# Kernel tuning notes

Hardware: AMD Instinct MI355X
Metric: run time of the kernel (lower is better)

## Reference

```python
import jax, jax.numpy as jnp
import numpy as np

NEG_SLOPE = 0.2
LN_EPS = 1e-5


def gat_conv(x, edge_index, W, att_src, att_dst, bias, heads, out_ch, concat):
    """PyG-style GATConv with add_self_loops=True, eval mode (no dropout)."""
    N = x.shape[0]
    loop = jnp.arange(N, dtype=edge_index.dtype)
    src = jnp.concatenate([edge_index[0], loop])
    dst = jnp.concatenate([edge_index[1], loop])
    h = (x @ W).reshape(N, heads, out_ch)                      # [N,H,C]
    a_src = jnp.sum(h * att_src, axis=-1)                      # [N,H]
    a_dst = jnp.sum(h * att_dst, axis=-1)                      # [N,H]
    e = jax.nn.leaky_relu(a_src[src] + a_dst[dst], NEG_SLOPE)  # [E,H]
    emax = jax.ops.segment_max(e, dst, num_segments=N)         # [N,H]
    ex = jnp.exp(e - emax[dst])
    denom = jax.ops.segment_sum(ex, dst, num_segments=N)       # [N,H]
    alpha = ex / denom[dst]                                    # [E,H]
    msg = h[src] * alpha[..., None]                            # [E,H,C]
    out = jax.ops.segment_sum(msg, dst, num_segments=N)        # [N,H,C]
    out = out.reshape(N, heads * out_ch) if concat else out.mean(axis=1)
    return out + bias


def layer_norm(x, w, b):
    mu = x.mean(-1, keepdims=True)
    var = jnp.mean((x - mu) ** 2, -1, keepdims=True)
    return (x - mu) * jax.lax.rsqrt(var + LN_EPS) * w + b


def setup_inputs() -> dict:
    key = jax.random.key(0)
    ks = jax.random.split(key, 16)
    N, E, R = 50000, 800000, 16
    node_dim, res_dim, hidden, heads = 128, 64, 64, 2
    s = lambda fan: 1.0 / np.sqrt(fan)
    return {
        "x": jax.random.normal(ks[0], (N, node_dim), jnp.float32),
        "edge_index": jax.random.randint(ks[1], (2, E), 0, N, jnp.int64),
        "resource_features": jax.random.normal(ks[2], (N, R, res_dim), jnp.float32),
        "W1": jax.random.normal(ks[3], (node_dim, heads * hidden), jnp.float32) * s(node_dim),
        "att_src1": jax.random.normal(ks[4], (heads, hidden), jnp.float32) * s(hidden),
        "att_dst1": jax.random.normal(ks[5], (heads, hidden), jnp.float32) * s(hidden),
        "b1": jnp.zeros((heads * hidden,), jnp.float32),
        "W2": jax.random.normal(ks[6], (heads * hidden, hidden), jnp.float32) * s(heads * hidden),
        "att_src2": jax.random.normal(ks[7], (1, hidden), jnp.float32) * s(hidden),
        "att_dst2": jax.random.normal(ks[8], (1, hidden), jnp.float32) * s(hidden),
        "b2": jnp.zeros((hidden,), jnp.float32),
        "ln_w": jnp.ones((hidden,), jnp.float32),
        "ln_b": jnp.zeros((hidden,), jnp.float32),
        "res_W": jax.random.normal(ks[9], (res_dim, hidden), jnp.float32) * s(res_dim),
        "res_b": jnp.zeros((hidden,), jnp.float32),
    }


def reference(x, edge_index, resource_features, W1, att_src1, att_dst1, b1,
              W2, att_src2, att_dst2, b2, ln_w, ln_b, res_W, res_b):
    hidden = W2.shape[1]
    heads = att_src1.shape[0]
    h = jax.nn.elu(gat_conv(x, edge_index, W1, att_src1, att_dst1, b1,
                            heads, hidden, concat=True))
    h = gat_conv(h, edge_index, W2, att_src2, att_dst2, b2,
                 1, hidden, concat=False)
    h = layer_norm(h, ln_w, ln_b)                              # [N, hidden]
    R = resource_features.shape[1]
    x_expanded = jnp.broadcast_to(h[:, None, :], (h.shape[0], R, hidden))
    res_emb = jax.nn.elu(resource_features @ res_W + res_b)    # [N,R,hidden]
    return jnp.concatenate([x_expanded, res_emb], axis=-1)     # [N,R,2*hidden]
```

## Files before the change

kernel.cpp:

```cpp
#include <hip/hip_runtime.h>
#include <hip/hip_bf16.h>
#include <math.h>

#define LEAKY_SLOPE 0.2f
#define LN_EPS 1e-5f

typedef __attribute__((ext_vector_type(4))) float f32x4;
typedef __attribute__((ext_vector_type(8))) short short8;

__device__ __forceinline__ float leaky_relu(float x) { return x >= 0.f ? x : LEAKY_SLOPE * x; }
__device__ __forceinline__ float elu1(float x) { return x > 0.f ? x : expm1f(x); }
__device__ __forceinline__ short f2bf(float f) {
    union { __hip_bfloat16 b; short s; } u;
    u.b = __float2bfloat16(f);
    return u.s;
}
__device__ __forceinline__ float bflo(unsigned u) { union { unsigned i; float f; } x; x.i = u << 16; return x.f; }
__device__ __forceinline__ float bfhi(unsigned u) { union { unsigned i; float f; } x; x.i = u & 0xffff0000u; return x.f; }
__device__ __forceinline__ float sbf(short s) { union { unsigned i; float f; } x; x.i = ((unsigned)(unsigned short)s) << 16; return x.f; }
__device__ __forceinline__ unsigned fkey(float f) {
    unsigned b = __float_as_uint(f);
    return b ^ (unsigned)(((int)b >> 31) | 0x80000000);
}
__device__ __forceinline__ float funkey(unsigned k) {
    unsigned b = (k & 0x80000000u) ? (k ^ 0x80000000u) : ~k;
    return __uint_as_float(b);
}

#define DETECT_IS64(ei, E)                                              \
    __shared__ int s_is64;                                              \
    {                                                                   \
        if (threadIdx.x < 64) {                                         \
            int v = (threadIdx.x < (E)) ? ((const int*)(ei))[2 * threadIdx.x + 1] : 0; \
            unsigned long long b = __ballot(v != 0);                    \
            if (threadIdx.x == 0) s_is64 = (b == 0ULL);                 \
        }                                                               \
        __syncthreads();                                                \
    }

#define SUBW1 130
#define DEGB 512
__global__ __launch_bounds__(256) void k_fat1(
    const float* __restrict__ x, const float* __restrict__ W1,
    const float* __restrict__ att_s, const float* __restrict__ att_d,
    short* __restrict__ h1, float* __restrict__ a_src, float* __restrict__ a_dst,
    unsigned* __restrict__ amax, int N,
    const void* __restrict__ ei, int E, int* __restrict__ deg, int nbG)
{
    if ((int)blockIdx.x >= nbG) {
        DETECT_IS64(ei, E)
        const int is64 = s_is64;
        const int b0 = (int)blockIdx.x - nbG;
        for (int e = b0 * 256 + threadIdx.x; e < E; e += DEGB * 256) {
            int d = is64 ? (int)((const long long*)ei)[(size_t)E + e] : ((const int*)ei)[(size_t)E + e];
            atomicAdd(&deg[d], 1);
        }
        return;
    }
    __shared__ short WT[16 * SUBW1 * 8];
    __shared__ float sb[64 * 4];
    __shared__ float wm[8];
    const int t = threadIdx.x;
    const int w = t >> 6, l = t & 63, lr = l & 15, lk = l >> 4;
    const int n0 = blockIdx.x * 64;
    for (int idx = t; idx < 16384; idx += 256) {
        int k = idx >> 7, col = idx & 127;
        WT[((k >> 3) * SUBW1 + col) * 8 + (k & 7)] = f2bf(W1[idx]);
    }
    sb[t] = 0.f;
    __syncthreads();

    f32x4 acc[4][2];
    #pragma unroll
    for (int mt = 0; mt < 4; ++mt)
        #pragma unroll
        for (int nt = 0; nt < 2; ++nt) acc[mt][nt] = (f32x4){0.f, 0.f, 0.f, 0.f};

    #pragma unroll
    for (int ks = 0; ks < 4; ++ks) {
        short8 bfr[2];
        #pragma unroll
        for (int nt = 0; nt < 2; ++nt) {
            int col = w * 32 + nt * 16 + lr;
            int kk = ks * 4 + lk;
            bfr[nt] = *(const short8*)&WT[(kk * SUBW1 + col) * 8];
        }
        #pragma unroll
        for (int mt = 0; mt < 4; ++mt) {
            int row = n0 + mt * 16 + lr; if (row >= N) row = N - 1;
            const float* ap = x + (size_t)row * 128 + ks * 32 + lk * 8;
            float4 u0 = *(const float4*)ap;
            float4 u1 = *(const float4*)(ap + 4);
            short8 af;
            af[0] = f2bf(u0.x); af[1] = f2bf(u0.y); af[2] = f2bf(u0.z); af[3] = f2bf(u0.w);
            af[4] = f2bf(u1.x); af[5] = f2bf(u1.y); af[6] = f2bf(u1.z); af[7] = f2bf(u1.w);
            acc[mt][0] = __builtin_amdgcn_mfma_f32_16x16x32_bf16(af, bfr[0], acc[mt][0], 0, 0, 0);
            acc[mt][1] = __builtin_amdgcn_mfma_f32_16x16x32_bf16(af, bfr[1], acc[mt][1], 0, 0, 0);
        }
    }

    const int head = w >> 1;
    float asv[2], adv[2];
    #pragma unroll
    for (int nt = 0; nt < 2; ++nt) {
        int ci = (w & 1) * 32 + nt * 16 + lr;
        asv[nt] = att_s[head * 64 + ci];
        adv[nt] = att_d[head * 64 + ci];
    }
    #pragma unroll
    for (int mt = 0; mt < 4; ++mt) {
        #pragma unroll
        for (int i = 0; i < 4; ++i) {
            float ps = acc[mt][0][i] * asv[0] + acc[mt][1][i] * asv[1];
            float pd = acc[mt][0][i] * adv[0] + acc[mt][1][i] * adv[1];
            #pragma unroll
            for (int o = 1; o < 16; o <<= 1) { ps += __shfl_xor(ps, o); pd += __shfl_xor(pd, o); }
            int rl = mt * 16 + lk * 4 + i;
            if (lr == 0) {
                atomicAdd(&sb[rl * 4 + head], ps);
                atomicAdd(&sb[rl * 4 + 2 + head], pd);
            }
            int row = n0 + rl;
            if (row < N) {
                h1[(size_t)row * 128 + w * 32 + lr]      = f2bf(acc[mt][0][i]);
                h1[(size_t)row * 128 + w * 32 + 16 + lr] = f2bf(acc[mt][1][i]);
            }
        }
    }
    __syncthreads();
    int nl = t >> 2, q = t & 3, n = n0 + nl;
    float v = sb[t];
    bool ok = (n < N);
    if (ok) {
        if (q == 0) a_src[n * 2 + 0] = v;
        else if (q == 1) a_src[n * 2 + 1] = v;
        else if (q == 2) a_dst[n * 2 + 0] = v;
        else a_dst[n * 2 + 1] = v;
    }
    float m0 = (ok && q == 0) ? v : -1e30f;
    float m1 = (ok && q == 1) ? v : -1e30f;
    #pragma unroll
    for (int o = 32; o; o >>= 1) { m0 = fmaxf(m0, __shfl_xor(m0, o)); m1 = fmaxf(m1, __shfl_xor(m1, o)); }
    if (l == 0) { wm[w] = m0; wm[4 + w] = m1; }
    __syncthreads();
    if (t == 0) {
        float M0 = fmaxf(fmaxf(wm[0], wm[1]), fmaxf(wm[2], wm[3]));
        float M1 = fmaxf(fmaxf(wm[4], wm[5]), fmaxf(wm[6], wm[7]));
        atomicMax(&amax[0], fkey(M0));
        atomicMax(&amax[1], fkey(M1));
    }
}

__global__ __launch_bounds__(256) void k_bsum(const int* __restrict__ deg, int* __restrict__ bsum, int n)
{
    __shared__ int ws[4];
    const int base = blockIdx.x * 1024;
    int s = 0;
    for (int j = threadIdx.x; j < 1024; j += 256) {
        int i = base + j;
        s += (i < n) ? deg[i] : 0;
    }
    #pragma unroll
    for (int o = 32; o; o >>= 1) s += __shfl_down(s, o);
    if ((threadIdx.x & 63) == 0) ws[threadIdx.x >> 6] = s;
    __syncthreads();
    if (threadIdx.x == 0) bsum[blockIdx.x] = ws[0] + ws[1] + ws[2] + ws[3];
}

__global__ void k_scanb(const int* __restrict__ bsum, int* __restrict__ bbase, int nb)
{
    const int l = threadIdx.x;
    int carry = 0;
    for (int b = 0; b < nb; b += 64) {
        int v = (b + l < nb) ? bsum[b + l] : 0;
        int x = v;
        #pragma unroll
        for (int o = 1; o < 64; o <<= 1) { int y = __shfl_up(x, o); if (l >= o) x += y; }
        if (b + l < nb) bbase[b + l] = carry + x - v;
        carry += __shfl(x, 63);
    }
}

__global__ __launch_bounds__(1024) void k_scan3(const int* __restrict__ deg, const int* __restrict__ bbase,
                                                int* __restrict__ offs, int* __restrict__ cursor, int n)
{
    __shared__ int ws[16];
    const int i = blockIdx.x * 1024 + threadIdx.x;
    const int l = threadIdx.x & 63, w = threadIdx.x >> 6;
    int v = (i < n) ? deg[i] : 0;
    int x = v;
    #pragma unroll
    for (int o = 1; o < 64; o <<= 1) { int y = __shfl_up(x, o); if (l >= o) x += y; }
    if (l == 63) ws[w] = x;
    __syncthreads();
    if (threadIdx.x < 16) {
        int s = ws[threadIdx.x];
        #pragma unroll
        for (int o = 1; o < 16; o <<= 1) { int y = __shfl_up(s, o); if (threadIdx.x >= o) s += y; }
        ws[threadIdx.x] = s;
    }
    __syncthreads();
    int add = (w ? ws[w - 1] : 0) + bbase[blockIdx.x];
    if (i < n) {
        offs[i + 1] = x + add;
        cursor[i] = x + add - v;
    }
    if (blockIdx.x == 0 && threadIdx.x == 0) offs[0] = 0;
}

__global__ __launch_bounds__(256) void k_scatter(const void* __restrict__ ei, int E,
                                                 int* __restrict__ cursor, int* __restrict__ csr_src)
{
    DETECT_IS64(ei, E)
    const int is64 = s_is64;
    for (int e = blockIdx.x * blockDim.x + threadIdx.x; e < E; e += gridDim.x * blockDim.x) {
        int s, d;
        if (is64) {
            const long long* p = (const long long*)ei;
            s = (int)p[e]; d = (int)p[(size_t)E + e];
        } else {
            const int* p = (const int*)ei;
            s = p[e]; d = p[(size_t)E + e];
        }
        int pos = atomicAdd(&cursor[d], 1);
        csr_src[pos] = s;
    }
}

__global__ __launch_bounds__(256) void k_layer1(
    const short* __restrict__ h1, const float* __restrict__ a_s, const float* __restrict__ a_d,
    const int* __restrict__ offs, const int* __restrict__ csr,
    const float* __restrict__ b1, const unsigned* __restrict__ amax,
    short* __restrict__ h1a, int N)
{
    const int w = threadIdx.x >> 6, l = threadIdx.x & 63;
    const int n = blockIdx.x * 4 + w;
    if (n >= N) return;
    const float2 adp = *(const float2*)&a_d[2 * n];
    const float2 asp = *(const float2*)&a_s[2 * n];
    const float C0 = leaky_relu(funkey(amax[0]) + adp.x);
    const float C1 = leaky_relu(funkey(amax[1]) + adp.y);
    const float es0 = leaky_relu(asp.x + adp.x) - C0;
    const float es1 = leaky_relu(asp.y + adp.y) - C1;
    const int hsel = l >> 5;
    const int o0 = offs[n], o1 = offs[n + 1];

    float den0 = 0.f, den1 = 0.f;
    float cl0 = 0.f, ch0 = 0.f, cl1 = 0.f, ch1 = 0.f;
    float cl2 = 0.f, ch2 = 0.f, cl3 = 0.f, ch3 = 0.f;
    for (int base = o0; base < o1; base += 64) {
        const int cnt = min(64, o1 - base);
        int sidx = 0; float p0 = 0.f, p1 = 0.f;
        if (l < cnt) {
            sidx = csr[base + l];
            float2 av = *(const float2*)&a_s[2 * sidx];
            p0 = __expf(leaky_relu(av.x + adp.x) - C0);
            p1 = __expf(leaky_relu(av.y + adp.y) - C1);
        }
        den0 += p0; den1 += p1;
        int j = 0;
        for (; j + 4 <= cnt; j += 4) {
            int s0 = __shfl(sidx, j),     s1 = __shfl(sidx, j + 1);
            int s2 = __shfl(sidx, j + 2), s3 = __shfl(sidx, j + 3);
            float q00 = __shfl(p0, j),     q10 = __shfl(p1, j);
            float q01 = __shfl(p0, j + 1), q11 = __shfl(p1, j + 1);
            float q02 = __shfl(p0, j + 2), q12 = __shfl(p1, j + 2);
            float q03 = __shfl(p0, j + 3), q13 = __shfl(p1, j + 3);
            unsigned u0 = *(const unsigned*)(h1 + (size_t)s0 * 128 + 2 * l);
            unsigned u1 = *(const unsigned*)(h1 + (size_t)s1 * 128 + 2 * l);
            unsigned u2 = *(const unsigned*)(h1 + (size_t)s2 * 128 + 2 * l);
            unsigned u3 = *(const unsigned*)(h1 + (size_t)s3 * 128 + 2 * l);
            float w0 = hsel ? q10 : q00, w1 = hsel ? q11 : q01;
            float w2 = hsel ? q12 : q02, w3 = hsel ? q13 : q03;
            cl0 += w0 * bflo(u0); ch0 += w0 * bfhi(u0);
            cl1 += w1 * bflo(u1); ch1 += w1 * bfhi(u1);
            cl2 += w2 * bflo(u2); ch2 += w2 * bfhi(u2);
            cl3 += w3 * bflo(u3); ch3 += w3 * bfhi(u3);
        }
        for (; j < cnt; ++j) {
            int sa = __shfl(sidx, j);
            float qa0 = __shfl(p0, j), qa1 = __shfl(p1, j);
            unsigned ua = *(const unsigned*)(h1 + (size_t)sa * 128 + 2 * l);
            float wa = hsel ? qa1 : qa0;
            cl0 += wa * bflo(ua); ch0 += wa * bfhi(ua);
        }
    }
    #pragma unroll
    for (int o = 32; o; o >>= 1) { den0 += __shfl_xor(den0, o); den1 += __shfl_xor(den1, o); }
    const float psf0 = __expf(es0), psf1 = __expf(es1);
    const float inv0 = 1.f / (den0 + psf0), inv1 = 1.f / (den1 + psf1);

    unsigned us = *(const unsigned*)(h1 + (size_t)n * 128 + 2 * l);
    const float psf = hsel ? psf1 : psf0;
    float acc0 = cl0 + cl1 + cl2 + cl3 + psf * bflo(us);
    float acc1 = ch0 + ch1 + ch2 + ch3 + psf * bfhi(us);
    const float invh = hsel ? inv1 : inv0;
    float2 bv = *(const float2*)&b1[2 * l];
    float v0 = elu1(acc0 * invh + bv.x);
    float v1 = elu1(acc1 * invh + bv.y);
    unsigned up = ((unsigned)(unsigned short)f2bf(v0)) | (((unsigned)(unsigned short)f2bf(v1)) << 16);
    *(unsigned*)(h1a + (size_t)n * 128 + 2 * l) = up;
}

#define SUBW2 66
__global__ __launch_bounds__(256) void k_gemm2m(
    const short* __restrict__ h1a, const float* __restrict__ W2,
    const float* __restrict__ att_s, const float* __restrict__ att_d,
    short* __restrict__ h2, float* __restrict__ a_src, float* __restrict__ a_dst,
    unsigned* __restrict__ amax, int N)
{
    __shared__ short WT[16 * SUBW2 * 8];
    __shared__ float sb[64 * 2];
    __shared__ float wm[4];
    const int t = threadIdx.x;
    const int w = t >> 6, l = t & 63, lr = l & 15, lk = l >> 4;
    const int n0 = blockIdx.x * 64;
    for (int idx = t; idx < 8192; idx += 256) {
        int k = idx >> 6, col = idx & 63;
        WT[((k >> 3) * SUBW2 + col) * 8 + (k & 7)] = f2bf(W2[idx]);
    }
    if (t < 128) sb[t] = 0.f;
    __syncthreads();

    f32x4 acc[4];
    #pragma unroll
    for (int mt = 0; mt < 4; ++mt) acc[mt] = (f32x4){0.f, 0.f, 0.f, 0.f};

    #pragma unroll
    for (int ks = 0; ks < 4; ++ks) {
        short8 bfr = *(const short8*)&WT[((ks * 4 + lk) * SUBW2 + w * 16 + lr) * 8];
        #pragma unroll
        for (int mt = 0; mt < 4; ++mt) {
            int row = n0 + mt * 16 + lr; if (row >= N) row = N - 1;
            short8 af = *(const short8*)(h1a + (size_t)row * 128 + ks * 32 + lk * 8);
            acc[mt] = __builtin_amdgcn_mfma_f32_16x16x32_bf16(af, bfr, acc[mt], 0, 0, 0);
        }
    }

    const float asv = att_s[w * 16 + lr], adv = att_d[w * 16 + lr];
    #pragma unroll
    for (int mt = 0; mt < 4; ++mt) {
        #pragma unroll
        for (int i = 0; i < 4; ++i) {
            float ps = acc[mt][i] * asv;
            float pd = acc[mt][i] * adv;
            #pragma unroll
            for (int o = 1; o < 16; o <<= 1) { ps += __shfl_xor(ps, o); pd += __shfl_xor(pd, o); }
            int rl = mt * 16 + lk * 4 + i;
            if (lr == 0) {
                atomicAdd(&sb[rl * 2 + 0], ps);
                atomicAdd(&sb[rl * 2 + 1], pd);
            }
            int row = n0 + rl;
            if (row < N) h2[(size_t)row * 64 + w * 16 + lr] = f2bf(acc[mt][i]);
        }
    }
    __syncthreads();
    float v = (t < 128) ? sb[t] : -1e30f;
    int n = n0 + (t >> 1);
    bool ok = (t < 128) && (n < N);
    if (ok) {
        if (t & 1) a_dst[n] = v;
        else       a_src[n] = v;
    }
    float m0 = (ok && !(t & 1)) ? v : -1e30f;
    #pragma unroll
    for (int o = 32; o; o >>= 1) m0 = fmaxf(m0, __shfl_xor(m0, o));
    if (l == 0) wm[w] = m0;
    __syncthreads();
    if (t == 0) {
        float M0 = fmaxf(fmaxf(wm[0], wm[1]), fmaxf(wm[2], wm[3]));
        atomicMax(&amax[0], fkey(M0));
    }
}

#define NPT 2
__global__ __launch_bounds__(256) void k_tail(
    const short* __restrict__ h2, const float* __restrict__ a_s, const float* __restrict__ a_d,
    const int* __restrict__ offs, const int* __restrict__ csr,
    const float* __restrict__ b2, const float* __restrict__ lnw, const float* __restrict__ lnb,
    const unsigned* __restrict__ amax,
    const float* __restrict__ res, const float* __restrict__ resW, const float* __restrict__ resb,
    float* __restrict__ out, int N)
{
    const int w = threadIdx.x >> 6, l = threadIdx.x & 63;
    const int lr = l & 15, lk = l >> 4;
    const int nbase = (blockIdx.x * 4 + w) * NPT;
    if (nbase >= N) return;

    short8 bf[2][4];
    #pragma unroll
    for (int kk = 0; kk < 2; ++kk)
        #pragma unroll
        for (int nc = 0; nc < 4; ++nc)
            #pragma unroll
            for (int j = 0; j < 8; ++j) {
                int k = kk * 32 + lk * 8 + j;
                bf[kk][nc][j] = f2bf(resW[k * 64 + nc * 16 + lr]);
            }
    float rbv[4];
    #pragma unroll
    for (int nc = 0; nc < 4; ++nc) rbv[nc] = resb[nc * 16 + lr];
    const float b2l = b2[l], lnwl = lnw[l], lnbl = lnb[l];
    const float Am = funkey(amax[0]);

    for (int i = 0; i < NPT; ++i) {
        const int n = nbase + i;
        if (n >= N) break;
        const float adv = a_d[n];
        const float C = leaky_relu(Am + adv);
        const float es = leaky_relu(a_s[n] + adv) - C;
        const int o0 = offs[n], o1 = offs[n + 1];
        float den = 0.f, a0 = 0.f, a1 = 0.f, a2 = 0.f, a3 = 0.f;
        for (int base = o0; base < o1; base += 64) {
            const int cnt = min(64, o1 - base);
            int sidx = 0; float pv = 0.f;
            if (l < cnt) {
                sidx = csr[base + l];
                pv = __expf(leaky_relu(a_s[sidx] + adv) - C);
            }
            den += pv;
            int j = 0;
            for (; j + 4 <= cnt; j += 4) {
                int s0 = __shfl(sidx, j),     s1 = __shfl(sidx, j + 1);
                int s2 = __shfl(sidx, j + 2), s3 = __shfl(sidx, j + 3);
                float q0 = __shfl(pv, j),     q1 = __shfl(pv, j + 1);
                float q2 = __shfl(pv, j + 2), q3 = __shfl(pv, j + 3);
                a0 += q0 * sbf(h2[(size_t)s0 * 64 + l]);
                a1 += q1 * sbf(h2[(size_t)s1 * 64 + l]);
                a2 += q2 * sbf(h2[(size_t)s2 * 64 + l]);
                a3 += q3 * sbf(h2[(size_t)s3 * 64 + l]);
            }
            for (; j < cnt; ++j) {
                int sa = __shfl(sidx, j);
                float qa = __shfl(pv, j);
                a0 += qa * sbf(h2[(size_t)sa * 64 + l]);
            }
        }
        #pragma unroll
        for (int o = 32; o; o >>= 1) den += __shfl_xor(den, o);
        const float psf = __expf(es);
        const float inv = 1.f / (den + psf);
        float o = (a0 + a1 + a2 + a3 + psf * sbf(h2[(size_t)n * 64 + l])) * inv + b2l;
        float mu = o;
        #pragma unroll
        for (int off = 32; off; off >>= 1) mu += __shfl_xor(mu, off);
        mu *= (1.f / 64.f);
        float d = o - mu;
        float vv = d * d;
        #pragma unroll
        for (int off = 32; off; off >>= 1) vv += __shfl_xor(vv, off);
        vv *= (1.f / 64.f);
        const float hl = d * rsqrtf(vv + LN_EPS) * lnwl + lnbl;
        f32x4 hv;
        #pragma unroll
        for (int j = 0; j < 4; ++j) hv[j] = __shfl(hl, lr * 4 + j);
        const float* rp = res + (size_t)n * 1024 + lr * 64 + lk * 8;
        const f32x4 f0 = __builtin_nontemporal_load((const f32x4*)(rp));
        const f32x4 f1 = __builtin_nontemporal_load((const f32x4*)(rp + 4));
        const f32x4 f2 = __builtin_nontemporal_load((const f32x4*)(rp + 32));
        const f32x4 f3 = __builtin_nontemporal_load((const f32x4*)(rp + 36));

        short8 fa0, fa1;
        fa0[0] = f2bf(f0[0]); fa0[1] = f2bf(f0[1]); fa0[2] = f2bf(f0[2]); fa0[3] = f2bf(f0[3]);
        fa0[4] = f2bf(f1[0]); fa0[5] = f2bf(f1[1]); fa0[6] = f2bf(f1[2]); fa0[7] = f2bf(f1[3]);
        fa1[0] = f2bf(f2[0]); fa1[1] = f2bf(f2[1]); fa1[2] = f2bf(f2[2]); fa1[3] = f2bf(f2[3]);
        fa1[4] = f2bf(f3[0]); fa1[5] = f2bf(f3[1]); fa1[6] = f2bf(f3[2]); fa1[7] = f2bf(f3[3]);

        f32x4 acc[4];
        #pragma unroll
        for (int nc = 0; nc < 4; ++nc) {
            acc[nc] = (f32x4){0.f, 0.f, 0.f, 0.f};
            acc[nc] = __builtin_amdgcn_mfma_f32_16x16x32_bf16(fa0, bf[0][nc], acc[nc], 0, 0, 0);
            acc[nc] = __builtin_amdgcn_mfma_f32_16x16x32_bf16(fa1, bf[1][nc], acc[nc], 0, 0, 0);
        }

        float* ob = out + (size_t)n * 2048;
        #pragma unroll
        for (int ii = 0; ii < 4; ++ii)
            __builtin_nontemporal_store(hv, (f32x4*)(ob + (lk + 4 * ii) * 128 + lr * 4));
        #pragma unroll
        for (int nc = 0; nc < 4; ++nc)
            #pragma unroll
            for (int ii = 0; ii < 4; ++ii) {
                float v = acc[nc][ii] + rbv[nc];
                __builtin_nontemporal_store(elu1(v), ob + (lk * 4 + ii) * 128 + 64 + nc * 16 + lr);
            }
    }
}

extern "C" void kernel_launch(void* const* d_in, const int* in_sizes, int n_in,
                              void* d_out, int out_size, void* d_ws, size_t ws_size,
                              hipStream_t stream)
{
    const float* x   = (const float*)d_in[0];
    const void*  ei  = d_in[1];
    const float* res = (const float*)d_in[2];
    const float* W1  = (const float*)d_in[3];
    const float* as1 = (const float*)d_in[4];
    const float* ad1 = (const float*)d_in[5];
    const float* b1  = (const float*)d_in[6];
    const float* W2  = (const float*)d_in[7];
    const float* as2 = (const float*)d_in[8];
    const float* ad2 = (const float*)d_in[9];
    const float* b2  = (const float*)d_in[10];
    const float* lnw = (const float*)d_in[11];
    const float* lnb = (const float*)d_in[12];
    const float* rW  = (const float*)d_in[13];
    const float* rb  = (const float*)d_in[14];
    float* out = (float*)d_out;

    const int N = in_sizes[0] / 128;
    const int E = in_sizes[1] / 2;
    const int nb = (N + 1023) / 1024;
    const int nbG = (N + 63) / 64;

    char* base = (char*)d_ws;
    size_t off = 0;
    auto alloc = [&](size_t bytes) -> void* {
        void* p = base + off;
        off = (off + bytes + 255) & ~(size_t)255;
        return p;
    };
    short* h1    = (short*)alloc((size_t)N * 128 * 2);
    short* h1a   = (short*)alloc((size_t)N * 128 * 2);
    short* h2    = (short*)alloc((size_t)N * 64 * 2);
    float* a_s1  = (float*)alloc((size_t)N * 2 * 4);
    float* a_d1  = (float*)alloc((size_t)N * 2 * 4);
    float* a_s2  = (float*)alloc((size_t)N * 4);
    float* a_d2  = (float*)alloc((size_t)N * 4);
    int* deg     = (int*)alloc((size_t)(N + 8) * 4);
    int* offs    = (int*)alloc((size_t)(N + 1) * 4);
    int* cursor  = (int*)alloc((size_t)N * 4);
    int* csr_src = (int*)alloc((size_t)E * 4);
    int* bsum    = (int*)alloc((size_t)nb * 4);
    int* bbase   = (int*)alloc((size_t)nb * 4);
    unsigned* amax1 = (unsigned*)(deg + N);
    unsigned* amax2 = (unsigned*)(deg + N + 2);

    (void)hipMemsetAsync(deg, 0, (size_t)(N + 8) * 4, stream);
    k_fat1<<<nbG + DEGB, 256, 0, stream>>>(x, W1, as1, ad1, h1, a_s1, a_d1, amax1, N, ei, E, deg, nbG);
    k_bsum<<<nb, 256, 0, stream>>>(deg, bsum, N);
    k_scanb<<<1, 64, 0, stream>>>(bsum, bbase, nb);
    k_scan3<<<nb, 1024, 0, stream>>>(deg, bbase, offs, cursor, N);
    k_scatter<<<512, 256, 0, stream>>>(ei, E, cursor, csr_src);
    k_layer1<<<(N + 3) / 4, 256, 0, stream>>>(h1, a_s1, a_d1, offs, csr_src, b1, amax1, h1a, N);
    k_gemm2m<<<(N + 63) / 64, 256, 0, stream>>>(h1a, W2, as2, ad2, h2, a_s2, a_d2, amax2, N);
    k_tail<<<(N + NPT * 4 - 1) / (NPT * 4), 256, 0, stream>>>(h2, a_s2, a_d2, offs, csr_src, b2, lnw, lnb,
                                                              amax2, res, rW, rb, out, N);
}
```

Baseline: 364.0 us.

## Move resource-embedding GEMM into layer-1 aggregation kernel with pre-swizzled bf16 weights

The resource_features @ res_W + ELU branch moves out of the tail kernel and into k_layer1, one node per wave. Each wave computes its node's 16x64 embedding with MFMA and writes the second half of the output. res_W is converted once to bf16 in the MFMA fragment layout by an extra block of k_fat1 and stored in the workspace, so the tail no longer builds per-lane fragments. The aim is to overlap the large streaming read of resource features with the latency-bound gather in layer 1 and to lighten the tail. The cost is more register pressure and memory traffic inside k_layer1, which may lower its occupancy.

```diff
diff --git a/kernel.cpp b/kernel.cpp
--- a/kernel.cpp
+++ b/kernel.cpp
@@ -45,12 +45,22 @@
     const float* __restrict__ att_s, const float* __restrict__ att_d,
     short* __restrict__ h1, float* __restrict__ a_src, float* __restrict__ a_dst,
     unsigned* __restrict__ amax, int N,
-    const void* __restrict__ ei, int E, int* __restrict__ deg, int nbG)
+    const void* __restrict__ ei, int E, int* __restrict__ deg,
+    const float* __restrict__ resW, short* __restrict__ rwb, int nbG)
 {
     if ((int)blockIdx.x >= nbG) {
+        const int b0 = (int)blockIdx.x - nbG;
+        if (b0 == 0) {
+            for (int idx = threadIdx.x; idx < 4096; idx += 256) {
+                int f = idx >> 9, lane = (idx >> 3) & 63, j = idx & 7;
+                int kk = f >> 2, nc = f & 3;
+                int k = kk * 32 + (lane >> 4) * 8 + j;
+                int col = nc * 16 + (lane & 15);
+                rwb[idx] = f2bf(resW[k * 64 + col]);
+            }
+        }
         DETECT_IS64(ei, E)
         const int is64 = s_is64;
-        const int b0 = (int)blockIdx.x - nbG;
         for (int e = b0 * 256 + threadIdx.x; e < E; e += DEGB * 256) {
             int d = is64 ? (int)((const long long*)ei)[(size_t)E + e] : ((const int*)ei)[(size_t)E + e];
             atomicAdd(&deg[d], 1);
@@ -231,7 +241,9 @@
     const short* __restrict__ h1, const float* __restrict__ a_s, const float* __restrict__ a_d,
     const int* __restrict__ offs, const int* __restrict__ csr,
     const float* __restrict__ b1, const unsigned* __restrict__ amax,
-    short* __restrict__ h1a, int N)
+    short* __restrict__ h1a, int N,
+    const float* __restrict__ res, const short* __restrict__ rwb,
+    const float* __restrict__ resb, float* __restrict__ out)
 {
     const int w = threadIdx.x >> 6, l = threadIdx.x & 63;
     const int n = blockIdx.x * 4 + w;
@@ -300,6 +312,33 @@
     float v1 = elu1(acc1 * invh + bv.y);
     unsigned up = ((unsigned)(unsigned short)f2bf(v0)) | (((unsigned)(unsigned short)f2bf(v1)) << 16);
     *(unsigned*)(h1a + (size_t)n * 128 + 2 * l) = up;
+
+    __builtin_amdgcn_sched_barrier(0);
+    {
+        const int lr = l & 15, lk = l >> 4;
+        const float* rp = res + (size_t)n * 1024 + lr * 64 + lk * 8;
+        const f32x4 f0 = __builtin_nontemporal_load((const f32x4*)(rp));
+        const f32x4 f1 = __builtin_nontemporal_load((const f32x4*)(rp + 4));
+        const f32x4 f2 = __builtin_nontemporal_load((const f32x4*)(rp + 32));
+        const f32x4 f3 = __builtin_nontemporal_load((const f32x4*)(rp + 36));
+        short8 fa0, fa1;
+        fa0[0] = f2bf(f0[0]); fa0[1] = f2bf(f0[1]); fa0[2] = f2bf(f0[2]); fa0[3] = f2bf(f0[3]);
+        fa0[4] = f2bf(f1[0]); fa0[5] = f2bf(f1[1]); fa0[6] = f2bf(f1[2]); fa0[7] = f2bf(f1[3]);
+        fa1[0] = f2bf(f2[0]); fa1[1] = f2bf(f2[1]); fa1[2] = f2bf(f2[2]); fa1[3] = f2bf(f2[3]);
+        fa1[4] = f2bf(f3[0]); fa1[5] = f2bf(f3[1]); fa1[6] = f2bf(f3[2]); fa1[7] = f2bf(f3[3]);
+        const short8* rw8 = (const short8*)rwb;
+        float* ob = out + (size_t)n * 2048;
+        #pragma unroll
+        for (int nc = 0; nc < 4; ++nc) {
+            f32x4 a = (f32x4){0.f, 0.f, 0.f, 0.f};
+            a = __builtin_amdgcn_mfma_f32_16x16x32_bf16(fa0, rw8[nc * 64 + l], a, 0, 0, 0);
+            a = __builtin_amdgcn_mfma_f32_16x16x32_bf16(fa1, rw8[(4 + nc) * 64 + l], a, 0, 0, 0);
+            const float rb = resb[nc * 16 + lr];
+            #pragma unroll
+            for (int ii = 0; ii < 4; ++ii)
+                __builtin_nontemporal_store(elu1(a[ii] + rb), ob + (lk * 4 + ii) * 128 + 64 + nc * 16 + lr);
+        }
+    }
 }
 
 #define SUBW2 66
@@ -379,28 +418,12 @@
     const short* __restrict__ h2, const float* __restrict__ a_s, const float* __restrict__ a_d,
     const int* __restrict__ offs, const int* __restrict__ csr,
     const float* __restrict__ b2, const float* __restrict__ lnw, const float* __restrict__ lnb,
-    const unsigned* __restrict__ amax,
-    const float* __restrict__ res, const float* __restrict__ resW, const float* __restrict__ resb,
-    float* __restrict__ out, int N)
+    const unsigned* __restrict__ amax, float* __restrict__ out, int N)
 {
     const int w = threadIdx.x >> 6, l = threadIdx.x & 63;
     const int lr = l & 15, lk = l >> 4;
     const int nbase = (blockIdx.x * 4 + w) * NPT;
     if (nbase >= N) return;
-
-    short8 bf[2][4];
-    #pragma unroll
-    for (int kk = 0; kk < 2; ++kk)
-        #pragma unroll
-        for (int nc = 0; nc < 4; ++nc)
-            #pragma unroll
-            for (int j = 0; j < 8; ++j) {
-                int k = kk * 32 + lk * 8 + j;
-                bf[kk][nc][j] = f2bf(resW[k * 64 + nc * 16 + lr]);
-            }
-    float rbv[4];
-    #pragma unroll
-    for (int nc = 0; nc < 4; ++nc) rbv[nc] = resb[nc * 16 + lr];
     const float b2l = b2[l], lnwl = lnw[l], lnbl = lnb[l];
     const float Am = funkey(amax[0]);
 
@@ -455,37 +478,10 @@
         f32x4 hv;
         #pragma unroll
         for (int j = 0; j < 4; ++j) hv[j] = __shfl(hl, lr * 4 + j);
-        const float* rp = res + (size_t)n * 1024 + lr * 64 + lk * 8;
-        const f32x4 f0 = __builtin_nontemporal_load((const f32x4*)(rp));
-        const f32x4 f1 = __builtin_nontemporal_load((const f32x4*)(rp + 4));
-        const f32x4 f2 = __builtin_nontemporal_load((const f32x4*)(rp + 32));
-        const f32x4 f3 = __builtin_nontemporal_load((const f32x4*)(rp + 36));
-
-        short8 fa0, fa1;
-        fa0[0] = f2bf(f0[0]); fa0[1] = f2bf(f0[1]); fa0[2] = f2bf(f0[2]); fa0[3] = f2bf(f0[3]);
-        fa0[4] = f2bf(f1[0]); fa0[5] = f2bf(f1[1]); fa0[6] = f2bf(f1[2]); fa0[7] = f2bf(f1[3]);
-        fa1[0] = f2bf(f2[0]); fa1[1] = f2bf(f2[1]); fa1[2] = f2bf(f2[2]); fa1[3] = f2bf(f2[3]);
-        fa1[4] = f2bf(f3[0]); fa1[5] = f2bf(f3[1]); fa1[6] = f2bf(f3[2]); fa1[7] = f2bf(f3[3]);
-
-        f32x4 acc[4];
-        #pragma unroll
-        for (int nc = 0; nc < 4; ++nc) {
-            acc[nc] = (f32x4){0.f, 0.f, 0.f, 0.f};
-            acc[nc] = __builtin_amdgcn_mfma_f32_16x16x32_bf16(fa0, bf[0][nc], acc[nc], 0, 0, 0);
-            acc[nc] = __builtin_amdgcn_mfma_f32_16x16x32_bf16(fa1, bf[1][nc], acc[nc], 0, 0, 0);
-        }
-
         float* ob = out + (size_t)n * 2048;
         #pragma unroll
         for (int ii = 0; ii < 4; ++ii)
             __builtin_nontemporal_store(hv, (f32x4*)(ob + (lk + 4 * ii) * 128 + lr * 4));
-        #pragma unroll
-        for (int nc = 0; nc < 4; ++nc)
-            #pragma unroll
-            for (int ii = 0; ii < 4; ++ii) {
-                float v = acc[nc][ii] + rbv[nc];
-                __builtin_nontemporal_store(elu1(v), ob + (lk * 4 + ii) * 128 + 64 + nc * 16 + lr);
-            }
     }
 }
 
@@ -535,17 +531,19 @@
     int* csr_src = (int*)alloc((size_t)E * 4);
     int* bsum    = (int*)alloc((size_t)nb * 4);
     int* bbase   = (int*)alloc((size_t)nb * 4);
+    short* rwb   = (short*)alloc(4096 * 2);
     unsigned* amax1 = (unsigned*)(deg + N);
     unsigned* amax2 = (unsigned*)(deg + N + 2);
 
     (void)hipMemsetAsync(deg, 0, (size_t)(N + 8) * 4, stream);
-    k_fat1<<<nbG + DEGB, 256, 0, stream>>>(x, W1, as1, ad1, h1, a_s1, a_d1, amax1, N, ei, E, deg, nbG);
+    k_fat1<<<nbG + DEGB, 256, 0, stream>>>(x, W1, as1, ad1, h1, a_s1, a_d1, amax1, N, ei, E, deg, rW, rwb, nbG);
     k_bsum<<<nb, 256, 0, stream>>>(deg, bsum, N);
     k_scanb<<<1, 64, 0, stream>>>(bsum, bbase, nb);
     k_scan3<<<nb, 1024, 0, stream>>>(deg, bbase, offs, cursor, N);
     k_scatter<<<512, 256, 0, stream>>>(ei, E, cursor, csr_src);
-    k_layer1<<<(N + 3) / 4, 256, 0, stream>>>(h1, a_s1, a_d1, offs, csr_src, b1, amax1, h1a, N);
+    k_layer1<<<(N + 3) / 4, 256, 0, stream>>>(h1, a_s1, a_d1, offs, csr_src, b1, amax1, h1a, N,
+                                              res, rwb, rb, out);
     k_gemm2m<<<(N + 63) / 64, 256, 0, stream>>>(h1a, W2, as2, ad2, h2, a_s2, a_d2, amax2, N);
     k_tail<<<(N + NPT * 4 - 1) / (NPT * 4), 256, 0, stream>>>(h2, a_s2, a_d2, offs, csr_src, b2, lnw, lnb,
-                                                              amax2, res, rW, rb, out, N);
-}
+                                                              amax2, out, N);
+}
```

Result: faster. 344.7 us (-5.3%).
